# Kernel optimization log

Measured on AMD Instinct MI355X. Metric: run time of the kernel, lower is better.

Reference implementation:

```python
import jax, jax.numpy as jnp
import numpy as np

NUM_HEADS = 4
NUM_GROUPS = 8
EPS = 1e-5


def group_norm(x, w, b):
    # x: (B, C, H, W); normalize per group of C//NUM_GROUPS channels
    B, C, H, W = x.shape
    xg = x.reshape(B, NUM_GROUPS, C // NUM_GROUPS, H, W)
    mean = xg.mean(axis=(2, 3, 4), keepdims=True)
    var = xg.var(axis=(2, 3, 4), keepdims=True)
    xn = ((xg - mean) * jax.lax.rsqrt(var + EPS)).reshape(B, C, H, W)
    return xn * w[None, :, None, None] + b[None, :, None, None]


def conv1x1(x, w, b):
    # x: (B, C_in, H, W), w: (C_out, C_in), b: (C_out,)
    return jnp.einsum('bchw,oc->bohw', x, w) + b[None, :, None, None]


def setup_inputs() -> dict:
    key = jax.random.key(0)
    B, C, H, W = 4, 256, 64, 64
    k1, k2, k3 = jax.random.split(key, 3)
    scale = 1.0 / np.sqrt(C)
    return {
        'x': jax.random.normal(k1, (B, C, H, W), dtype=jnp.float32),
        'norm_w': jnp.ones((C,), dtype=jnp.float32),
        'norm_b': jnp.zeros((C,), dtype=jnp.float32),
        'qkv_w': jax.random.normal(k2, (3 * C, C), dtype=jnp.float32) * scale,
        'qkv_b': jnp.zeros((3 * C,), dtype=jnp.float32),
        'proj_w': jax.random.normal(k3, (C, C), dtype=jnp.float32) * scale,
        'proj_b': jnp.zeros((C,), dtype=jnp.float32),
    }


def reference(x, norm_w, norm_b, qkv_w, qkv_b, proj_w, proj_b):
    B, C, H, W = x.shape
    hd = C // NUM_HEADS  # head dim
    h = group_norm(x, norm_w, norm_b)
    qkv = conv1x1(h, qkv_w, qkv_b)            # (B, 3C, H, W)
    q, k, v = jnp.split(qkv, 3, axis=1)
    q = q.reshape(B, NUM_HEADS, hd, H * W)
    k = k.reshape(B, NUM_HEADS, hd, H * W)
    v = v.reshape(B, NUM_HEADS, hd, H * W)
    attn = jnp.einsum('bhcn,bhcm->bhnm', q, k) / jnp.sqrt(jnp.asarray(hd, x.dtype))
    attn = jax.nn.softmax(attn, axis=-1)
    out = jnp.einsum('bhnm,bhcm->bhcn', attn, v).reshape(B, C, H, W)
    out = conv1x1(out, proj_w, proj_b)
    return x + out
```

## Files before the change

kernel.cpp:

```cpp
#include <hip/hip_runtime.h>
#include <hip/hip_bf16.h>
#include <stdint.h>


#define B_  4
#define C_  256
#define N_  4096
#define NH_ 4
#define HD_ 64
#define G_  8
#define CPG_ 32
#define GRP_ELEMS (CPG_ * N_)

typedef __attribute__((ext_vector_type(8))) short short8;
typedef __attribute__((ext_vector_type(4))) float f32x4;
typedef __attribute__((ext_vector_type(4))) unsigned short us4;

__device__ __forceinline__ unsigned short f2bf(float f) {
  union { float f; unsigned u; } v; v.f = f;
  unsigned r = v.u + 0x7FFFu + ((v.u >> 16) & 1u);
  return (unsigned short)(r >> 16);
}

__device__ __forceinline__ unsigned pkbf2(float a, float b) {
  __hip_bfloat162 h = __float22bfloat162_rn(make_float2(a, b));
  unsigned r; __builtin_memcpy(&r, &h, sizeof(r)); return r;
}

__device__ __forceinline__ void dma16(const unsigned short* g, unsigned short* l) {
  __builtin_amdgcn_global_load_lds(
      (const __attribute__((address_space(1))) unsigned int*)(g),
      (__attribute__((address_space(3))) unsigned int*)(l), 16, 0, 0);
}

__global__ void cvt_weights(const float* __restrict__ qkvw,
                            const float* __restrict__ projw,
                            unsigned short* __restrict__ wq,
                            unsigned short* __restrict__ wp) {
  int i = blockIdx.x * 256 + threadIdx.x;
  if (i < 768 * 256) wq[i] = f2bf(qkvw[i]);
  if (i < 256 * 256) wp[i] = f2bf(projw[i]);
}

__global__ void gn_partial(const float* __restrict__ x, float* __restrict__ partial) {
  int idx = blockIdx.x;
  int slice = idx & 15, g = (idx >> 4) & 7, b = idx >> 7;
  int t = threadIdx.x;
  const float* base = x + (size_t)(b * C_ + g * CPG_) * N_ + slice * 256;
  float s = 0.f, sq = 0.f;
#pragma unroll
  for (int cc = 0; cc < CPG_; cc++) {
    float v = base[(size_t)cc * N_ + t];
    s += v; sq += v * v;
  }
#pragma unroll
  for (int off = 32; off; off >>= 1) {
    s  += __shfl_down(s,  off, 64);
    sq += __shfl_down(sq, off, 64);
  }
  __shared__ float ls[8];
  int wave = t >> 6, lane = t & 63;
  if (lane == 0) { ls[wave * 2] = s; ls[wave * 2 + 1] = sq; }
  __syncthreads();
  if (t == 0) {
    float S = ls[0] + ls[2] + ls[4] + ls[6];
    float SQ = ls[1] + ls[3] + ls[5] + ls[7];
    partial[idx * 2] = S; partial[idx * 2 + 1] = SQ;
  }
}

__global__ void gn_finalize(const float* __restrict__ partial, float* __restrict__ stats) {
  int t = threadIdx.x;
  if (t < 32) {
    float s = 0.f, sq = 0.f;
    for (int i = 0; i < 16; i++) {
      s  += partial[(t * 16 + i) * 2];
      sq += partial[(t * 16 + i) * 2 + 1];
    }
    const float inv = 1.0f / (float)GRP_ELEMS;
    float mean = s * inv;
    float var = sq * inv - mean * mean;
    stats[t * 2] = mean;
    stats[t * 2 + 1] = rsqrtf(var + 1e-5f);
  }
}

__global__ void gn_apply(const float* __restrict__ x,
                         const float* __restrict__ nw, const float* __restrict__ nb,
                         const float* __restrict__ stats, unsigned short* __restrict__ hT) {
  int nt = blockIdx.x, ct = blockIdx.y, b = blockIdx.z;
  __shared__ unsigned short tile[32][72];
  int t = threadIdx.x;
  int n_loc = t & 63, c_loc = t >> 6;
  float mean = stats[(b * G_ + ct) * 2];
  float rstd = stats[(b * G_ + ct) * 2 + 1];
  const float* xb = x + (size_t)(b * C_ + ct * CPG_) * N_ + nt * 64;
#pragma unroll
  for (int rr = 0; rr < 8; rr++) {
    int cc = rr * 4 + c_loc;
    int c = ct * CPG_ + cc;
    float v = xb[(size_t)cc * N_ + n_loc];
    v = (v - mean) * rstd * nw[c] + nb[c];
    tile[cc][n_loc] = f2bf(v);
  }
  __syncthreads();
  int c2 = t & 31, n2 = t >> 5;
  unsigned short* out = hT + ((size_t)(b * N_ + nt * 64)) * C_ + ct * CPG_ + c2;
#pragma unroll
  for (int pass = 0; pass < 8; pass++) {
    int n = pass * 8 + n2;
    out[(size_t)n * C_] = tile[c2][n];
  }
}

__global__ __launch_bounds__(256) void qkv_gemm(
    const unsigned short* __restrict__ hT, const unsigned short* __restrict__ wq,
    const float* __restrict__ qb,
    unsigned short* __restrict__ Qt, unsigned short* __restrict__ Kt,
    unsigned short* __restrict__ V) {
  int nt = blockIdx.x, ot = blockIdx.y, b = blockIdx.z;
  int t = threadIdx.x;
  int wave = t >> 6, lane = t & 63, l15 = lane & 15, quad = lane >> 4, l7 = l15 & 7;
  int o_base = ot * 64 + wave * 16;

  __shared__ __align__(16) unsigned short sh[64 * C_];

  {
    int row0 = wave * 2 + (lane >> 5);
    int col8 = lane & 31;
    int src8 = (col8 & 24) | ((col8 & 7) ^ (row0 & 7));
    const unsigned short* gsrc = hT + ((size_t)(b * N_ + nt * 64 + row0)) * C_ + src8 * 8;
#pragma unroll
    for (int it = 0; it < 8; it++)
      dma16(gsrc + (size_t)it * 8 * C_, sh + (it * 8 + wave * 2) * C_);
  }

  f32x4 acc[4];
#pragma unroll
  for (int tt = 0; tt < 4; tt++) acc[tt] = (f32x4){0.f, 0.f, 0.f, 0.f};

  const short8* arow = reinterpret_cast<const short8*>(wq + (size_t)(o_base + l15) * C_);

  asm volatile("s_waitcnt vmcnt(0)" ::: "memory");
  __syncthreads();

#pragma unroll
  for (int kk = 0; kk < 8; kk++) {
    short8 a = arow[kk * 4 + quad];
    int g = kk * 4 + quad;
    int col8 = (g & 24) | ((g & 7) ^ l7);
#pragma unroll
    for (int tt = 0; tt < 4; tt++) {
      short8 bf = *reinterpret_cast<const short8*>(&sh[(tt * 16 + l15) * C_ + col8 * 8]);
      acc[tt] = __builtin_amdgcn_mfma_f32_16x16x32_bf16(a, bf, acc[tt], 0, 0, 0);
    }
  }

  int sec = ot >> 2, head = ot & 3;
  int cw = wave * 16 + quad * 4;
  int bh = b * NH_ + head;
  const float SC = 0.125f * 1.44269504088896340736f;

  if (sec == 0) {
#pragma unroll
    for (int tt = 0; tt < 4; tt++) {
      int n = nt * 64 + tt * 16 + l15;
      us4 pk;
#pragma unroll
      for (int i = 0; i < 4; i++)
        pk[i] = f2bf((acc[tt][i] + qb[ot * 64 + cw + i]) * SC);
      *reinterpret_cast<us4*>(Qt + ((size_t)bh * N_ + n) * HD_ + cw) = pk;
    }
  } else if (sec == 1) {
#pragma unroll
    for (int tt = 0; tt < 4; tt++) {
      int n = nt * 64 + tt * 16 + l15;
      us4 pk;
#pragma unroll
      for (int i = 0; i < 4; i++)
        pk[i] = f2bf(acc[tt][i] + qb[ot * 64 + cw + i]);
      *reinterpret_cast<us4*>(Kt + ((size_t)bh * N_ + n) * HD_ + cw) = pk;
    }
  } else {
#pragma unroll
    for (int tt = 0; tt < 4; tt++) {
      int n = nt * 64 + tt * 16 + l15;
#pragma unroll
      for (int i = 0; i < 4; i++)
        V[((size_t)bh * HD_ + cw + i) * N_ + n] = f2bf(acc[tt][i] + qb[ot * 64 + cw + i]);
    }
  }
}

__global__ __launch_bounds__(256, 2) void flash_attn(
    const unsigned short* __restrict__ Qt, const unsigned short* __restrict__ Kt,
    const unsigned short* __restrict__ Vv, unsigned short* __restrict__ aoT) {
  int bh = blockIdx.x & 15, qt = blockIdx.x >> 4;
  int b = bh >> 2, head = bh & 3;
  int t = threadIdx.x;
  int wave = t >> 6, lane = t & 63, l15 = lane & 15, quad = lane >> 4;
  int l7 = l15 & 7;
  int qsub = wave >> 1, khalf = wave & 1;

  const unsigned short* Qb = Qt + (size_t)bh * N_ * HD_;
  const unsigned short* Kb = Kt + (size_t)bh * N_ * HD_;
  const unsigned short* Vb = Vv + (size_t)bh * HD_ * N_;
  int q_base = qt * 128 + qsub * 64;

  __shared__ __align__(16) unsigned char smem[74752];
  unsigned short* Ks = (unsigned short*)smem;
  unsigned short* Vs = (unsigned short*)(smem + 32768);
  unsigned short* Ps = (unsigned short*)(smem + 65536);
  float* Obuf = (float*)smem;
  float* lbuf = (float*)(smem + 34816);

  const short8 vones = {(short)0x3F80, (short)0x3F80, (short)0x3F80, (short)0x3F80,
                        (short)0x3F80, (short)0x3F80, (short)0x3F80, (short)0x3F80};

  short8 qf[4][2];
#pragma unroll
  for (int r = 0; r < 4; r++)
#pragma unroll
    for (int h = 0; h < 2; h++)
      qf[r][h] = *reinterpret_cast<const short8*>(
          Qb + (size_t)(q_base + r * 16 + l15) * HD_ + h * 32 + quad * 8);

  f32x4 oa[4][4], la[4];
#pragma unroll
  for (int r = 0; r < 4; r++) {
    la[r] = (f32x4){0.f, 0.f, 0.f, 0.f};
#pragma unroll
    for (int ct = 0; ct < 4; ct++) oa[r][ct] = (f32x4){0.f, 0.f, 0.f, 0.f};
  }

  int i8 = lane >> 3, e = lane & 7;
  int perm = (e ^ i8) * 8;
  int kvoff = (khalf * 2) * 4096;
  auto stage = [&](int kt2, int buf) {
    int m0 = khalf * 2048 + kt2 * 64;
    unsigned short* Kd = Ks + kvoff + buf * 4096;
    unsigned short* Vd = Vs + kvoff + buf * 4096;
#pragma unroll
    for (int cc = 0; cc < 4; cc++) {
      int c = qsub * 4 + cc;
      dma16(Kb + (size_t)(m0 + c * 8 + i8) * HD_ + perm, Kd + c * 512);
      dma16(Vb + (size_t)(c * 8 + i8) * N_ + m0 + perm, Vd + c * 512);
    }
  };

  stage(0, 0);

  unsigned short* Pw = Ps + wave * 16 * 72;

#pragma unroll 1
  for (int kt = 0; kt < 32; kt++) {
    int buf = kt & 1;
    asm volatile("s_waitcnt vmcnt(0)" ::: "memory");
    __builtin_amdgcn_s_barrier();
    if (kt + 1 < 32) stage(kt + 1, buf ^ 1);

    const unsigned short* Kbuf = Ks + kvoff + buf * 4096;
    const unsigned short* Vbuf = Vs + kvoff + buf * 4096;

    short8 kf[4][2], vf[4][2];
#pragma unroll
    for (int tt = 0; tt < 4; tt++)
#pragma unroll
      for (int kh2 = 0; kh2 < 2; kh2++) {
        kf[tt][kh2] = *reinterpret_cast<const short8*>(
            &Kbuf[(tt * 16 + l15) * 64 + (((kh2 * 4 + quad) ^ l7) * 8)]);
        vf[tt][kh2] = *reinterpret_cast<const short8*>(
            &Vbuf[(tt * 16 + l15) * 64 + (((kh2 * 4 + quad) ^ l7) * 8)]);
      }

#pragma unroll
    for (int r = 0; r < 4; r++) {
      f32x4 s[4];
#pragma unroll
      for (int tt = 0; tt < 4; tt++) {
        f32x4 z = (f32x4){0.f, 0.f, 0.f, 0.f};
        z = __builtin_amdgcn_mfma_f32_16x16x32_bf16(kf[tt][0], qf[r][0], z, 0, 0, 0);
        s[tt] = __builtin_amdgcn_mfma_f32_16x16x32_bf16(kf[tt][1], qf[r][1], z, 0, 0, 0);
      }
#pragma unroll
      for (int tt = 0; tt < 4; tt++) {
        union { unsigned u2[2]; us4 v; } w;
        w.u2[0] = pkbf2(__builtin_amdgcn_exp2f(s[tt][0]), __builtin_amdgcn_exp2f(s[tt][1]));
        w.u2[1] = pkbf2(__builtin_amdgcn_exp2f(s[tt][2]), __builtin_amdgcn_exp2f(s[tt][3]));
        *reinterpret_cast<us4*>(&Pw[l15 * 72 + tt * 16 + quad * 4]) = w.v;
      }
      short8 pf0 = *reinterpret_cast<const short8*>(&Pw[l15 * 72 + quad * 8]);
      short8 pf1 = *reinterpret_cast<const short8*>(&Pw[l15 * 72 + 32 + quad * 8]);
#pragma unroll
      for (int ct = 0; ct < 4; ct++) {
        oa[r][ct] = __builtin_amdgcn_mfma_f32_16x16x32_bf16(vf[ct][0], pf0, oa[r][ct], 0, 0, 0);
        oa[r][ct] = __builtin_amdgcn_mfma_f32_16x16x32_bf16(vf[ct][1], pf1, oa[r][ct], 0, 0, 0);
      }
      la[r] = __builtin_amdgcn_mfma_f32_16x16x32_bf16(vones, pf0, la[r], 0, 0, 0);
      la[r] = __builtin_amdgcn_mfma_f32_16x16x32_bf16(vones, pf1, la[r], 0, 0, 0);
    }
  }

  __builtin_amdgcn_s_barrier();
  if (khalf == 1) {
#pragma unroll
    for (int r = 0; r < 4; r++) {
#pragma unroll
      for (int ct = 0; ct < 4; ct++)
#pragma unroll
        for (int i = 0; i < 4; i++)
          Obuf[qsub * 4352 + (ct * 16 + quad * 4 + i) * 68 + r * 16 + l15] = oa[r][ct][i];
      if (quad == 0) lbuf[qsub * 64 + r * 16 + l15] = la[r][0];
    }
  }
  __builtin_amdgcn_s_barrier();
  if (khalf == 0) {
#pragma unroll
    for (int r = 0; r < 4; r++) {
      float inv = 1.0f / (la[r][0] + lbuf[qsub * 64 + r * 16 + l15]);
      int n = q_base + r * 16 + l15;
#pragma unroll
      for (int ct = 0; ct < 4; ct++) {
        const float* ob = &Obuf[qsub * 4352 + (ct * 16 + quad * 4) * 68 + r * 16 + l15];
        union { unsigned u2[2]; us4 v; } w;
        w.u2[0] = pkbf2((oa[r][ct][0] + ob[0]) * inv, (oa[r][ct][1] + ob[68]) * inv);
        w.u2[1] = pkbf2((oa[r][ct][2] + ob[136]) * inv, (oa[r][ct][3] + ob[204]) * inv);
        *reinterpret_cast<us4*>(
            aoT + ((size_t)(b * N_ + n)) * C_ + head * HD_ + ct * 16 + quad * 4) = w.v;
      }
    }
  }
}

__global__ __launch_bounds__(256) void proj_gemm(
    const unsigned short* __restrict__ aoT, const unsigned short* __restrict__ wp,
    const float* __restrict__ pb, const float* __restrict__ x,
    float* __restrict__ out) {
  int nt = blockIdx.x, ot = blockIdx.y, b = blockIdx.z;
  int t = threadIdx.x;
  int wave = t >> 6, lane = t & 63, l15 = lane & 15, quad = lane >> 4, l7 = l15 & 7;
  int o_base = ot * 64 + wave * 16;

  __shared__ __align__(16) unsigned short sh[64 * C_];

  {
    int row0 = wave * 2 + (lane >> 5);
    int col8 = lane & 31;
    int src8 = (col8 & 24) | ((col8 & 7) ^ (row0 & 7));
    const unsigned short* gsrc = aoT + ((size_t)(b * N_ + nt * 64 + row0)) * C_ + src8 * 8;
#pragma unroll
    for (int it = 0; it < 8; it++)
      dma16(gsrc + (size_t)it * 8 * C_, sh + (it * 8 + wave * 2) * C_);
  }

  f32x4 acc[4];
#pragma unroll
  for (int tt = 0; tt < 4; tt++) acc[tt] = (f32x4){0.f, 0.f, 0.f, 0.f};

  const short8* arow = reinterpret_cast<const short8*>(wp + (size_t)(o_base + l15) * C_);

  asm volatile("s_waitcnt vmcnt(0)" ::: "memory");
  __syncthreads();

#pragma unroll
  for (int kk = 0; kk < 8; kk++) {
    short8 a = arow[kk * 4 + quad];
    int g = kk * 4 + quad;
    int col8 = (g & 24) | ((g & 7) ^ l7);
#pragma unroll
    for (int tt = 0; tt < 4; tt++) {
      short8 bf = *reinterpret_cast<const short8*>(&sh[(tt * 16 + l15) * C_ + col8 * 8]);
      acc[tt] = __builtin_amdgcn_mfma_f32_16x16x32_bf16(a, bf, acc[tt], 0, 0, 0);
    }
  }
#pragma unroll
  for (int tt = 0; tt < 4; tt++) {
    int n = nt * 64 + tt * 16 + l15;
#pragma unroll
    for (int i = 0; i < 4; i++) {
      int o = o_base + quad * 4 + i;
      size_t idx = ((size_t)(b * C_ + o)) * N_ + n;
      out[idx] = acc[tt][i] + pb[o] + x[idx];
    }
  }
}

extern "C" void kernel_launch(void* const* d_in, const int* in_sizes, int n_in,
                              void* d_out, int out_size, void* d_ws, size_t ws_size,
                              hipStream_t stream) {
  const float* x      = (const float*)d_in[0];
  const float* norm_w = (const float*)d_in[1];
  const float* norm_b = (const float*)d_in[2];
  const float* qkv_w  = (const float*)d_in[3];
  const float* qkv_b  = (const float*)d_in[4];
  const float* proj_w = (const float*)d_in[5];
  const float* proj_b = (const float*)d_in[6];
  float* out = (float*)d_out;

  char* ws = (char*)d_ws;
  size_t off = 0;
  auto alloc = [&](size_t bytes) { size_t o = off; off = (off + bytes + 255) & ~(size_t)255; return o; };
  size_t off_partial = alloc(512 * 2 * sizeof(float));
  size_t off_stats   = alloc(32 * 2 * sizeof(float));
  size_t off_wq      = alloc((size_t)768 * 256 * 2);
  size_t off_wp      = alloc((size_t)256 * 256 * 2);
  size_t off_hT      = alloc((size_t)B_ * N_ * C_ * 2);
  size_t off_Qt      = alloc((size_t)B_ * NH_ * N_ * HD_ * 2);
  size_t off_Kt      = alloc((size_t)B_ * NH_ * N_ * HD_ * 2);
  size_t off_V       = alloc((size_t)B_ * NH_ * HD_ * N_ * 2);
  size_t off_aoT     = alloc((size_t)B_ * N_ * C_ * 2);

  float* partial = (float*)(ws + off_partial);
  float* stats   = (float*)(ws + off_stats);
  unsigned short* wq  = (unsigned short*)(ws + off_wq);
  unsigned short* wp  = (unsigned short*)(ws + off_wp);
  unsigned short* hT  = (unsigned short*)(ws + off_hT);
  unsigned short* Qt  = (unsigned short*)(ws + off_Qt);
  unsigned short* Kt  = (unsigned short*)(ws + off_Kt);
  unsigned short* V   = (unsigned short*)(ws + off_V);
  unsigned short* aoT = (unsigned short*)(ws + off_aoT);

  cvt_weights<<<768, 256, 0, stream>>>(qkv_w, proj_w, wq, wp);
  gn_partial<<<512, 256, 0, stream>>>(x, partial);
  gn_finalize<<<1, 64, 0, stream>>>(partial, stats);
  gn_apply<<<dim3(64, 8, 4), 256, 0, stream>>>(x, norm_w, norm_b, stats, hT);
  qkv_gemm<<<dim3(64, 12, 4), 256, 0, stream>>>(hT, wq, qkv_b, Qt, Kt, V);
  flash_attn<<<512, 256, 0, stream>>>(Qt, Kt, V, aoT);
  proj_gemm<<<dim3(64, 4, 4), 256, 0, stream>>>(aoT, wp, proj_b, x, out);
}
```

Measured before the change: 200.8 us.

## Give each attention wave private K/V staging to drop per-iteration block barriers

The flash attention loop now stages K/V into a per-wave LDS region, 32 keys per step over 64 steps, instead of a block-shared 64-key tile synchronized with a block barrier every iteration. Each wave loads its own K and V slice with a new V swizzle and a narrower P buffer, so only vmcnt waits are needed inside the loop. This removes inter-wave barrier stalls. In exchange, the two waves sharing a query subtile each load the same K/V data, so global traffic doubles, and each wave runs twice as many iterations with smaller MFMA batches.

New measurement: 209.5 us. 4.3% more time.

```diff
diff --git a/kernel.cpp b/kernel.cpp
--- a/kernel.cpp
+++ b/kernel.cpp
@@ -124,7 +124,6 @@
   int o_base = ot * 64 + wave * 16;
 
   __shared__ __align__(16) unsigned short sh[64 * C_];
-
   {
     int row0 = wave * 2 + (lane >> 5);
     int col8 = lane & 31;
@@ -207,12 +206,12 @@
   const unsigned short* Vb = Vv + (size_t)bh * HD_ * N_;
   int q_base = qt * 128 + qsub * 64;
 
-  __shared__ __align__(16) unsigned char smem[74752];
-  unsigned short* Ks = (unsigned short*)smem;
-  unsigned short* Vs = (unsigned short*)(smem + 32768);
-  unsigned short* Ps = (unsigned short*)(smem + 65536);
-  float* Obuf = (float*)smem;
-  float* lbuf = (float*)(smem + 34816);
+  __shared__ __align__(16) unsigned char smem[72704];
+  unsigned short* Pw = (unsigned short*)(smem + 65536 + wave * 1792);
+  float* ObA = (float*)smem;
+  float* ObB = (float*)(smem + 17408);
+  float* lbA = (float*)(smem + 34816);
+  float* lbB = (float*)(smem + 35072);
 
   const short8 vones = {(short)0x3F80, (short)0x3F80, (short)0x3F80, (short)0x3F80,
                         (short)0x3F80, (short)0x3F80, (short)0x3F80, (short)0x3F80};
@@ -233,95 +232,99 @@
     for (int ct = 0; ct < 4; ct++) oa[r][ct] = (f32x4){0.f, 0.f, 0.f, 0.f};
   }
 
-  int i8 = lane >> 3, e = lane & 7;
-  int perm = (e ^ i8) * 8;
-  int kvoff = (khalf * 2) * 4096;
+  int i8 = lane >> 3, e8 = lane & 7;
+  int r16 = lane >> 2, e4 = lane & 3;
+  int kperm = (e8 ^ i8) * 8;
+  int vperm = (e4 ^ ((r16 >> 1) & 3)) * 8;
+
   auto stage = [&](int kt2, int buf) {
-    int m0 = khalf * 2048 + kt2 * 64;
-    unsigned short* Kd = Ks + kvoff + buf * 4096;
-    unsigned short* Vd = Vs + kvoff + buf * 4096;
+    int m0 = khalf * 2048 + kt2 * 32;
+    unsigned short* Kd = (unsigned short*)(smem + wave * 8192 + buf * 4096);
+    unsigned short* Vd = (unsigned short*)(smem + 32768 + wave * 8192 + buf * 4096);
 #pragma unroll
     for (int cc = 0; cc < 4; cc++) {
-      int c = qsub * 4 + cc;
-      dma16(Kb + (size_t)(m0 + c * 8 + i8) * HD_ + perm, Kd + c * 512);
-      dma16(Vb + (size_t)(c * 8 + i8) * N_ + m0 + perm, Vd + c * 512);
+      dma16(Kb + (size_t)(m0 + cc * 8 + i8) * HD_ + kperm, Kd + cc * 512);
+      dma16(Vb + (size_t)(cc * 16 + r16) * N_ + m0 + vperm, Vd + cc * 512);
     }
   };
 
   stage(0, 0);
 
-  unsigned short* Pw = Ps + wave * 16 * 72;
-
 #pragma unroll 1
-  for (int kt = 0; kt < 32; kt++) {
+  for (int kt = 0; kt < 64; kt++) {
     int buf = kt & 1;
     asm volatile("s_waitcnt vmcnt(0)" ::: "memory");
-    __builtin_amdgcn_s_barrier();
-    if (kt + 1 < 32) stage(kt + 1, buf ^ 1);
-
-    const unsigned short* Kbuf = Ks + kvoff + buf * 4096;
-    const unsigned short* Vbuf = Vs + kvoff + buf * 4096;
-
-    short8 kf[4][2], vf[4][2];
-#pragma unroll
-    for (int tt = 0; tt < 4; tt++)
-#pragma unroll
-      for (int kh2 = 0; kh2 < 2; kh2++) {
-        kf[tt][kh2] = *reinterpret_cast<const short8*>(
-            &Kbuf[(tt * 16 + l15) * 64 + (((kh2 * 4 + quad) ^ l7) * 8)]);
-        vf[tt][kh2] = *reinterpret_cast<const short8*>(
-            &Vbuf[(tt * 16 + l15) * 64 + (((kh2 * 4 + quad) ^ l7) * 8)]);
+    if (kt + 1 < 64) stage(kt + 1, buf ^ 1);
+
+    const unsigned short* Kw = (const unsigned short*)(smem + wave * 8192 + buf * 4096);
+    const unsigned short* Vw = (const unsigned short*)(smem + 32768 + wave * 8192 + buf * 4096);
+
+    short8 kf[2][2];
+#pragma unroll
+    for (int tt = 0; tt < 2; tt++)
+#pragma unroll
+      for (int kh = 0; kh < 2; kh++)
+        kf[tt][kh] = *reinterpret_cast<const short8*>(
+            &Kw[(tt * 16 + l15) * 64 + (((kh * 4 + quad) ^ l7) * 8)]);
+    short8 vf[4];
+#pragma unroll
+    for (int ct = 0; ct < 4; ct++)
+      vf[ct] = *reinterpret_cast<const short8*>(
+          &Vw[(ct * 16 + l15) * 32 + ((quad ^ ((l15 >> 1) & 3)) * 8)]);
+
+#pragma unroll
+    for (int r = 0; r < 4; r++) {
+      f32x4 s0, s1;
+      {
+        f32x4 z = (f32x4){0.f, 0.f, 0.f, 0.f};
+        z  = __builtin_amdgcn_mfma_f32_16x16x32_bf16(kf[0][0], qf[r][0], z, 0, 0, 0);
+        s0 = __builtin_amdgcn_mfma_f32_16x16x32_bf16(kf[0][1], qf[r][1], z, 0, 0, 0);
       }
-
+      {
+        f32x4 z = (f32x4){0.f, 0.f, 0.f, 0.f};
+        z  = __builtin_amdgcn_mfma_f32_16x16x32_bf16(kf[1][0], qf[r][0], z, 0, 0, 0);
+        s1 = __builtin_amdgcn_mfma_f32_16x16x32_bf16(kf[1][1], qf[r][1], z, 0, 0, 0);
+      }
+      union { unsigned u2[2]; us4 v; } w0, w1;
+      w0.u2[0] = pkbf2(__builtin_amdgcn_exp2f(s0[0]), __builtin_amdgcn_exp2f(s0[1]));
+      w0.u2[1] = pkbf2(__builtin_amdgcn_exp2f(s0[2]), __builtin_amdgcn_exp2f(s0[3]));
+      w1.u2[0] = pkbf2(__builtin_amdgcn_exp2f(s1[0]), __builtin_amdgcn_exp2f(s1[1]));
+      w1.u2[1] = pkbf2(__builtin_amdgcn_exp2f(s1[2]), __builtin_amdgcn_exp2f(s1[3]));
+      *reinterpret_cast<us4*>(&Pw[l15 * 56 + quad * 4]) = w0.v;
+      *reinterpret_cast<us4*>(&Pw[l15 * 56 + 16 + quad * 4]) = w1.v;
+      short8 pf = *reinterpret_cast<const short8*>(&Pw[l15 * 56 + quad * 8]);
+#pragma unroll
+      for (int ct = 0; ct < 4; ct++)
+        oa[r][ct] = __builtin_amdgcn_mfma_f32_16x16x32_bf16(vf[ct], pf, oa[r][ct], 0, 0, 0);
+      la[r] = __builtin_amdgcn_mfma_f32_16x16x32_bf16(vones, pf, la[r], 0, 0, 0);
+    }
+  }
+
+  __syncthreads();
+  if (khalf == 1) {
+    float* Ob = (qsub == 0) ? ObA : ObB;
+    float* lb = (qsub == 0) ? lbA : lbB;
 #pragma unroll
     for (int r = 0; r < 4; r++) {
-      f32x4 s[4];
-#pragma unroll
-      for (int tt = 0; tt < 4; tt++) {
-        f32x4 z = (f32x4){0.f, 0.f, 0.f, 0.f};
-        z = __builtin_amdgcn_mfma_f32_16x16x32_bf16(kf[tt][0], qf[r][0], z, 0, 0, 0);
-        s[tt] = __builtin_amdgcn_mfma_f32_16x16x32_bf16(kf[tt][1], qf[r][1], z, 0, 0, 0);
-      }
-#pragma unroll
-      for (int tt = 0; tt < 4; tt++) {
-        union { unsigned u2[2]; us4 v; } w;
-        w.u2[0] = pkbf2(__builtin_amdgcn_exp2f(s[tt][0]), __builtin_amdgcn_exp2f(s[tt][1]));
-        w.u2[1] = pkbf2(__builtin_amdgcn_exp2f(s[tt][2]), __builtin_amdgcn_exp2f(s[tt][3]));
-        *reinterpret_cast<us4*>(&Pw[l15 * 72 + tt * 16 + quad * 4]) = w.v;
-      }
-      short8 pf0 = *reinterpret_cast<const short8*>(&Pw[l15 * 72 + quad * 8]);
-      short8 pf1 = *reinterpret_cast<const short8*>(&Pw[l15 * 72 + 32 + quad * 8]);
+#pragma unroll
+      for (int ct = 0; ct < 4; ct++)
+#pragma unroll
+        for (int i = 0; i < 4; i++)
+          Ob[(ct * 16 + quad * 4 + i) * 68 + r * 16 + l15] = oa[r][ct][i];
+      if (quad == 0) lb[r * 16 + l15] = la[r][0];
+    }
+  }
+  __syncthreads();
+  if (khalf == 0) {
+    const float* Ob = (qsub == 0) ? ObA : ObB;
+    const float* lb = (qsub == 0) ? lbA : lbB;
+#pragma unroll
+    for (int r = 0; r < 4; r++) {
+      float inv = 1.0f / (la[r][0] + lb[r * 16 + l15]);
+      int n = q_base + r * 16 + l15;
 #pragma unroll
       for (int ct = 0; ct < 4; ct++) {
-        oa[r][ct] = __builtin_amdgcn_mfma_f32_16x16x32_bf16(vf[ct][0], pf0, oa[r][ct], 0, 0, 0);
-        oa[r][ct] = __builtin_amdgcn_mfma_f32_16x16x32_bf16(vf[ct][1], pf1, oa[r][ct], 0, 0, 0);
-      }
-      la[r] = __builtin_amdgcn_mfma_f32_16x16x32_bf16(vones, pf0, la[r], 0, 0, 0);
-      la[r] = __builtin_amdgcn_mfma_f32_16x16x32_bf16(vones, pf1, la[r], 0, 0, 0);
-    }
-  }
-
-  __builtin_amdgcn_s_barrier();
-  if (khalf == 1) {
-#pragma unroll
-    for (int r = 0; r < 4; r++) {
-#pragma unroll
-      for (int ct = 0; ct < 4; ct++)
-#pragma unroll
-        for (int i = 0; i < 4; i++)
-          Obuf[qsub * 4352 + (ct * 16 + quad * 4 + i) * 68 + r * 16 + l15] = oa[r][ct][i];
-      if (quad == 0) lbuf[qsub * 64 + r * 16 + l15] = la[r][0];
-    }
-  }
-  __builtin_amdgcn_s_barrier();
-  if (khalf == 0) {
-#pragma unroll
-    for (int r = 0; r < 4; r++) {
-      float inv = 1.0f / (la[r][0] + lbuf[qsub * 64 + r * 16 + l15]);
-      int n = q_base + r * 16 + l15;
-#pragma unroll
-      for (int ct = 0; ct < 4; ct++) {
-        const float* ob = &Obuf[qsub * 4352 + (ct * 16 + quad * 4) * 68 + r * 16 + l15];
+        const float* ob = &Ob[(ct * 16 + quad * 4) * 68 + r * 16 + l15];
         union { unsigned u2[2]; us4 v; } w;
         w.u2[0] = pkbf2((oa[r][ct][0] + ob[0]) * inv, (oa[r][ct][1] + ob[68]) * inv);
         w.u2[1] = pkbf2((oa[r][ct][2] + ob[136]) * inv, (oa[r][ct][3] + ob[204]) * inv);
@@ -342,7 +345,6 @@
   int o_base = ot * 64 + wave * 16;
 
   __shared__ __align__(16) unsigned short sh[64 * C_];
-
   {
     int row0 = wave * 2 + (lane >> 5);
     int col8 = lane & 31;
```
